# Kernel tuning notes

Hardware: AMD Instinct MI355X
Metric: run time of the kernel (lower is better)

## Reference

```python
import jax, jax.numpy as jnp
import numpy as np

EPS = 1e-08
STEPS_START = 0
STEPS_END = 500


def setup_inputs() -> dict:
    key = jax.random.key(0)
    k_x, k_w, k_beta, k_b = jax.random.split(key, 4)
    B, T, D_in, D_out = 64, 500, 1024, 128
    x = jax.random.normal(k_x, (B, T, D_in), dtype=jnp.float32)
    # w ~ N(w_init_mean, w_init_std * sqrt(1/input_shape))
    w = jax.random.normal(k_w, (D_in, D_out), dtype=jnp.float32) * np.sqrt(1.0 / D_in)
    beta = jax.random.uniform(k_beta, (D_out,), dtype=jnp.float32)  # clamped to [0,1] in torch
    b = jax.random.uniform(k_b, (D_out,), dtype=jnp.float32)        # clamped >= 0 in torch
    return {"x": x, "w": w, "beta": beta, "b": b}


def reference(x, w, beta, b):
    # x: [B, T, D_in], w: [D_in, D_out], beta/b: [D_out]
    h = jnp.einsum('btc,cd->btd', x, w)          # [B, T, D_out]
    norm = jnp.sum(w * w, axis=0)                # [D_out]

    one_minus_beta = 1.0 - beta

    def step(mem, h_t):
        mem = mem * beta + one_minus_beta * h_t  # Leaky_Neuron=True
        return mem, mem

    mem0 = jnp.zeros((x.shape[0], w.shape[1]), dtype=x.dtype)
    _, mem_rec = jax.lax.scan(step, mem0, jnp.swapaxes(h, 0, 1))  # [T, B, D_out]
    mem_rec = jnp.swapaxes(mem_rec, 0, 1)                          # [B, T, D_out]

    # time_reduction == 'mean'
    output = jnp.mean(mem_rec[:, STEPS_START:STEPS_END, :], axis=1) / (norm + EPS) - b
    return output
```

## Files before the change

### kernel.cpp

```cpp
#include <hip/hip_runtime.h>
#include <hip/hip_bf16.h>

#define B_    64
#define T_    500
#define DIN   1024
#define DOUT  128
#define EPSV  1e-8f
#define BM    128
#define BK    64
#define NKT   (DIN / BK)
#define TILES 4

typedef __attribute__((ext_vector_type(8))) short bf16x8;
typedef __attribute__((ext_vector_type(4))) float f32x4;

#define OFF_WTAB  262144
#define OFF_SCALE 518144
#define OFF_PART  518656

__device__ inline short f2bf(float f) {
    __hip_bfloat16 h = __float2bfloat16(f);
    return __builtin_bit_cast(short, h);
}

__global__ __launch_bounds__(256) void prep_kernel(
    const float* __restrict__ w, const float* __restrict__ beta,
    __hip_bfloat16* __restrict__ wT, float* __restrict__ wtab,
    float* __restrict__ scale)
{
    int bid = blockIdx.x, tid = threadIdx.x;
    if (bid < 512) {
        int i = bid * 256 + tid;
        int d = i >> 10, k = i & 1023;
        wT[(size_t)d * DIN + k] = __float2bfloat16(w[(size_t)k * DOUT + d]);
    } else if (bid < 640) {
        int d = bid - 512;
        __shared__ float red[256];
        float s = 0.f;
        for (int c = tid; c < DIN; c += 256) {
            float v = w[(size_t)c * DOUT + d];
            s += v * v;
        }
        red[tid] = s;
        __syncthreads();
        for (int off = 128; off > 0; off >>= 1) {
            if (tid < off) red[tid] += red[tid + off];
            __syncthreads();
        }
        if (tid == 0) scale[d] = 1.f / ((red[0] + EPSV) * (float)T_);
    } else {
        int i = (bid - 640) * 256 + tid;
        if (i < T_ * DOUT) {
            int t = i >> 7, d = i & 127;
            wtab[i] = 1.f - powf(beta[d], (float)(T_ - t));
        }
    }
}

__global__ __launch_bounds__(512, 2) void gemm_kernel(
    const float* __restrict__ x, const __hip_bfloat16* __restrict__ wT,
    const float* __restrict__ wtab, float* __restrict__ partials)
{
    __shared__ __align__(16) char smem[2 * 32768];

    const int wg   = blockIdx.x;
    const int tile = wg & 3;
    const int b    = wg >> 2;
    const int t0   = tile * BM;
    const int tid  = threadIdx.x;
    const int wid  = tid >> 6;
    const int lane = tid & 63;
    const int arow = lane & 15;
    const int kblk = lane >> 4;
    const int wr   = wid >> 2;
    const int wc   = wid & 3;

    const float* xb = x + (size_t)b * T_ * DIN;

    const int sr = tid >> 4;
    const int sc = tid & 15;
    const float* ag[4];
    int awoff[4];
#pragma unroll
    for (int p = 0; p < 4; ++p) {
        int row  = p * 32 + sr;
        int trow = t0 + row; if (trow >= T_) trow = T_ - 1;
        ag[p] = xb + (size_t)trow * DIN + sc * 4;
        awoff[p] = (row * 128 + sc * 8) ^ ((row & 7) << 4);
    }
    const int bcol = tid >> 2;
    const int bch0 = (tid & 3) * 2;
    const __hip_bfloat16* bg0 = wT + (size_t)bcol * DIN + bch0 * 8;
    const __hip_bfloat16* bg1 = bg0 + 8;
    const int bwoff0 = (bcol * 128 + bch0 * 16)        ^ ((bcol & 7) << 4);
    const int bwoff1 = (bcol * 128 + (bch0 + 1) * 16)  ^ ((bcol & 7) << 4);

    int aro[4][2], bro[2][2];
#pragma unroll
    for (int fm = 0; fm < 4; ++fm)
#pragma unroll
        for (int kk = 0; kk < 2; ++kk) {
            int row = wr * 64 + fm * 16 + arow;
            aro[fm][kk] = (row * 128 + kk * 64 + kblk * 16) ^ ((row & 7) << 4);
        }
#pragma unroll
    for (int fn = 0; fn < 2; ++fn)
#pragma unroll
        for (int kk = 0; kk < 2; ++kk) {
            int col = wc * 32 + fn * 16 + arow;
            bro[fn][kk] = (col * 128 + kk * 64 + kblk * 16) ^ ((col & 7) << 4);
        }

    f32x4 acc[4][2] = {};

    {
        char* Ab = smem;
        char* Bb = smem + 16384;
#pragma unroll
        for (int p = 0; p < 4; ++p) {
            float4 v = *reinterpret_cast<const float4*>(ag[p]);
            short4 h; h.x = f2bf(v.x); h.y = f2bf(v.y); h.z = f2bf(v.z); h.w = f2bf(v.w);
            *reinterpret_cast<short4*>(Ab + awoff[p]) = h;
        }
        *reinterpret_cast<bf16x8*>(Bb + bwoff0) = *reinterpret_cast<const bf16x8*>(bg0);
        *reinterpret_cast<bf16x8*>(Bb + bwoff1) = *reinterpret_cast<const bf16x8*>(bg1);
    }
    __syncthreads();

    for (int kt = 0; kt < NKT; ++kt) {
        const int cur = kt & 1;
        char* Acur = smem + cur * 32768;
        char* Bcur = Acur + 16384;
        char* Anxt = smem + (cur ^ 1) * 32768;
        char* Bnxt = Anxt + 16384;

        float4 av[4]; bf16x8 bv0, bv1;
        if (kt < NKT - 1) {
            const int kb = (kt + 1) * BK;
#pragma unroll
            for (int p = 0; p < 4; ++p)
                av[p] = *reinterpret_cast<const float4*>(ag[p] + kb);
            bv0 = *reinterpret_cast<const bf16x8*>(bg0 + kb);
            bv1 = *reinterpret_cast<const bf16x8*>(bg1 + kb);
        }

        bf16x8 af[4][2], bf[2][2];
#pragma unroll
        for (int fm = 0; fm < 4; ++fm)
#pragma unroll
            for (int kk = 0; kk < 2; ++kk)
                af[fm][kk] = *reinterpret_cast<const bf16x8*>(Acur + aro[fm][kk]);
#pragma unroll
        for (int fn = 0; fn < 2; ++fn)
#pragma unroll
            for (int kk = 0; kk < 2; ++kk)
                bf[fn][kk] = *reinterpret_cast<const bf16x8*>(Bcur + bro[fn][kk]);

#pragma unroll
        for (int kk = 0; kk < 2; ++kk)
#pragma unroll
            for (int fm = 0; fm < 4; ++fm)
#pragma unroll
                for (int fn = 0; fn < 2; ++fn)
                    acc[fm][fn] = __builtin_amdgcn_mfma_f32_16x16x32_bf16(
                        af[fm][kk], bf[fn][kk], acc[fm][fn], 0, 0, 0);

        if (kt < NKT - 1) {
#pragma unroll
            for (int p = 0; p < 4; ++p) {
                short4 h; h.x = f2bf(av[p].x); h.y = f2bf(av[p].y);
                h.z = f2bf(av[p].z); h.w = f2bf(av[p].w);
                *reinterpret_cast<short4*>(Anxt + awoff[p]) = h;
            }
            *reinterpret_cast<bf16x8*>(Bnxt + bwoff0) = bv0;
            *reinterpret_cast<bf16x8*>(Bnxt + bwoff1) = bv1;
        }
        __syncthreads();
    }

    const int col0 = wc * 32 + arow;
    const int col1 = col0 + 16;
    float s0 = 0.f, s1 = 0.f;
#pragma unroll
    for (int fm = 0; fm < 4; ++fm) {
#pragma unroll
        for (int r = 0; r < 4; ++r) {
            int t = t0 + wr * 64 + fm * 16 + kblk * 4 + r;
            if (t < T_) {
                s0 += wtab[t * DOUT + col0] * acc[fm][0][r];
                s1 += wtab[t * DOUT + col1] * acc[fm][1][r];
            }
        }
    }
    s0 += __shfl_xor(s0, 16); s0 += __shfl_xor(s0, 32);
    s1 += __shfl_xor(s1, 16); s1 += __shfl_xor(s1, 32);

    if (kblk == 0) {
        float* p = partials + (((size_t)b * TILES + tile) * 2 + wr) * DOUT;
        p[col0] = s0;
        p[col1] = s1;
    }
}

__global__ __launch_bounds__(256) void finalize_kernel(
    const float* __restrict__ partials, const float* __restrict__ scale,
    const float* __restrict__ bias, float* __restrict__ out)
{
    int i = blockIdx.x * 256 + threadIdx.x;
    int b = i >> 7, d = i & 127;
    float s = 0.f;
#pragma unroll
    for (int p = 0; p < TILES * 2; ++p)
        s += partials[((size_t)b * TILES * 2 + p) * DOUT + d];
    out[i] = s * scale[d] - bias[d];
}

extern "C" void kernel_launch(void* const* d_in, const int* in_sizes, int n_in,
                              void* d_out, int out_size, void* d_ws, size_t ws_size,
                              hipStream_t stream) {
    const float* x    = (const float*)d_in[0];
    const float* w    = (const float*)d_in[1];
    const float* beta = (const float*)d_in[2];
    const float* bias = (const float*)d_in[3];
    float* out = (float*)d_out;

    char* ws = (char*)d_ws;
    __hip_bfloat16* wT = (__hip_bfloat16*)(ws);
    float* wtab     = (float*)(ws + OFF_WTAB);
    float* scale    = (float*)(ws + OFF_SCALE);
    float* partials = (float*)(ws + OFF_PART);

    prep_kernel<<<890, 256, 0, stream>>>(w, beta, wT, wtab, scale);
    gemm_kernel<<<B_ * TILES, 512, 0, stream>>>(x, wT, wtab, partials);
    finalize_kernel<<<(B_ * DOUT) / 256, 256, 0, stream>>>(partials, scale, bias, out);
}
```

Measured before the change: 40.90 us.

## Split GEMM K dimension across two workgroups and raise occupancy

Splits the K reduction of the GEMM into two chunks handled by separate workgroups, doubling the grid from 256 to 512 blocks so more CUs are busy on a 256-CU part. Partial weighted sums per K chunk are written separately and summed in the finalize kernel. It also raises launch_bounds min blocks per SM to 4 and interleaves LDS fragment loads with MFMAs to reduce register pressure. The cost is twice the partial-sum traffic and a shorter per-block pipeline with more prologue overhead.

```diff
diff --git a/kernel.cpp b/kernel.cpp
--- a/kernel.cpp
+++ b/kernel.cpp
@@ -8,7 +8,9 @@
 #define EPSV  1e-8f
 #define BM    128
 #define BK    64
-#define NKT   (DIN / BK)
+#define NKC   2
+#define KCL   (DIN / NKC)
+#define NKT   (KCL / BK)
 #define TILES 4
 
 typedef __attribute__((ext_vector_type(8))) short bf16x8;
@@ -57,16 +59,18 @@
     }
 }
 
-__global__ __launch_bounds__(512, 2) void gemm_kernel(
+__global__ __launch_bounds__(512, 4) void gemm_kernel(
     const float* __restrict__ x, const __hip_bfloat16* __restrict__ wT,
     const float* __restrict__ wtab, float* __restrict__ partials)
 {
     __shared__ __align__(16) char smem[2 * 32768];
 
     const int wg   = blockIdx.x;
-    const int tile = wg & 3;
-    const int b    = wg >> 2;
+    const int kc   = wg & 1;
+    const int tile = (wg >> 1) & 3;
+    const int b    = wg >> 3;
     const int t0   = tile * BM;
+    const int kbase = kc * KCL;
     const int tid  = threadIdx.x;
     const int wid  = tid >> 6;
     const int lane = tid & 63;
@@ -75,7 +79,7 @@
     const int wr   = wid >> 2;
     const int wc   = wid & 3;
 
-    const float* xb = x + (size_t)b * T_ * DIN;
+    const float* xb = x + (size_t)b * T_ * DIN + kbase;
 
     const int sr = tid >> 4;
     const int sc = tid & 15;
@@ -90,7 +94,7 @@
     }
     const int bcol = tid >> 2;
     const int bch0 = (tid & 3) * 2;
-    const __hip_bfloat16* bg0 = wT + (size_t)bcol * DIN + bch0 * 8;
+    const __hip_bfloat16* bg0 = wT + (size_t)bcol * DIN + kbase + bch0 * 8;
     const __hip_bfloat16* bg1 = bg0 + 8;
     const int bwoff0 = (bcol * 128 + bch0 * 16)        ^ ((bcol & 7) << 4);
     const int bwoff1 = (bcol * 128 + (bch0 + 1) * 16)  ^ ((bcol & 7) << 4);
@@ -144,26 +148,17 @@
             bv1 = *reinterpret_cast<const bf16x8*>(bg1 + kb);
         }
 
-        bf16x8 af[4][2], bf[2][2];
-#pragma unroll
-        for (int fm = 0; fm < 4; ++fm)
-#pragma unroll
-            for (int kk = 0; kk < 2; ++kk)
-                af[fm][kk] = *reinterpret_cast<const bf16x8*>(Acur + aro[fm][kk]);
-#pragma unroll
-        for (int fn = 0; fn < 2; ++fn)
-#pragma unroll
-            for (int kk = 0; kk < 2; ++kk)
-                bf[fn][kk] = *reinterpret_cast<const bf16x8*>(Bcur + bro[fn][kk]);
-
-#pragma unroll
-        for (int kk = 0; kk < 2; ++kk)
-#pragma unroll
-            for (int fm = 0; fm < 4; ++fm)
-#pragma unroll
-                for (int fn = 0; fn < 2; ++fn)
-                    acc[fm][fn] = __builtin_amdgcn_mfma_f32_16x16x32_bf16(
-                        af[fm][kk], bf[fn][kk], acc[fm][fn], 0, 0, 0);
+#pragma unroll
+        for (int kk = 0; kk < 2; ++kk) {
+            bf16x8 bf0 = *reinterpret_cast<const bf16x8*>(Bcur + bro[0][kk]);
+            bf16x8 bf1 = *reinterpret_cast<const bf16x8*>(Bcur + bro[1][kk]);
+#pragma unroll
+            for (int fm = 0; fm < 4; ++fm) {
+                bf16x8 af = *reinterpret_cast<const bf16x8*>(Acur + aro[fm][kk]);
+                acc[fm][0] = __builtin_amdgcn_mfma_f32_16x16x32_bf16(af, bf0, acc[fm][0], 0, 0, 0);
+                acc[fm][1] = __builtin_amdgcn_mfma_f32_16x16x32_bf16(af, bf1, acc[fm][1], 0, 0, 0);
+            }
+        }
 
         if (kt < NKT - 1) {
 #pragma unroll
@@ -196,7 +191,7 @@
     s1 += __shfl_xor(s1, 16); s1 += __shfl_xor(s1, 32);
 
     if (kblk == 0) {
-        float* p = partials + (((size_t)b * TILES + tile) * 2 + wr) * DOUT;
+        float* p = partials + ((((size_t)b * TILES + tile) * 2 + wr) * NKC + kc) * DOUT;
         p[col0] = s0;
         p[col1] = s1;
     }
@@ -210,8 +205,8 @@
     int b = i >> 7, d = i & 127;
     float s = 0.f;
 #pragma unroll
-    for (int p = 0; p < TILES * 2; ++p)
-        s += partials[((size_t)b * TILES * 2 + p) * DOUT + d];
+    for (int p = 0; p < TILES * 2 * NKC; ++p)
+        s += partials[((size_t)b * TILES * 2 * NKC + p) * DOUT + d];
     out[i] = s * scale[d] - bias[d];
 }
 
@@ -231,6 +226,6 @@
     float* partials = (float*)(ws + OFF_PART);
 
     prep_kernel<<<890, 256, 0, stream>>>(w, beta, wT, wtab, scale);
-    gemm_kernel<<<B_ * TILES, 512, 0, stream>>>(x, wT, wtab, partials);
+    gemm_kernel<<<B_ * TILES * NKC, 512, 0, stream>>>(x, wT, wtab, partials);
     finalize_kernel<<<(B_ * DOUT) / 256, 256, 0, stream>>>(partials, scale, bias, out);
 }
```

Result: faster. 36.87 us (-9.9%).
